# Optimization experiments

Hardware: AMD Instinct MI355X
Metric: run time of the kernel (lower is better)

The kernel has to match this reference:

```python
import jax, jax.numpy as jnp
import numpy as np

P = 8192  # num_particles
C = 8192  # num EEG channels (must equal P for the original broadcast to be valid)


def setup_inputs() -> dict:
    key = jax.random.key(0)
    k1, k2, k3, k4, k5 = jax.random.split(key, 5)
    inputs = jax.random.normal(k1, (1, C, P), dtype=jnp.float32)
    state_vector = jax.random.normal(k2, (P, 3), dtype=jnp.float32)
    # near-identity transition for numerical sanity
    transition_matrix = jnp.eye(3, dtype=jnp.float32) + 0.01 * jax.random.normal(k3, (3, 3), dtype=jnp.float32)
    # symmetric positive-definite process noise covariance (Cholesky must succeed)
    a = jax.random.normal(k4, (3, 3), dtype=jnp.float32)
    process_noise_cov = 0.01 * (a @ a.T) + 0.1 * jnp.eye(3, dtype=jnp.float32)
    forward_matrix = jax.random.normal(k5, (C, 3), dtype=jnp.float32)
    return {
        "inputs": inputs,
        "state_vector": state_vector,
        "transition_matrix": transition_matrix,
        "process_noise_cov": process_noise_cov,
        "forward_matrix": forward_matrix,
    }


def reference(inputs, state_vector, transition_matrix, process_noise_cov, forward_matrix):
    k_noise, k_cat = jax.random.split(jax.random.key(42))
    # --- state transition: x_new = x @ T^T + eps,  eps ~ N(0, Q) via z @ chol(Q) ---
    updated = state_vector @ transition_matrix.T                      # (P, 3)
    L = jnp.linalg.cholesky(process_noise_cov)                        # (3, 3) lower
    z = jax.random.normal(k_noise, (P, 3), dtype=state_vector.dtype)
    state = updated + z @ L                                           # (P, 3)
    # --- EEG measurement model: H @ x^T -> (C, P) ---
    predicted = forward_matrix @ state.T                              # (C, P)
    # --- particle weights: squared-residual sum (broadcast (1,C,P) - (P,C), C==P) ---
    w = jnp.sum(jnp.square(inputs - predicted.T), axis=-1)[0]         # (P,)
    # --- categorical resampling on log-weights (unnormalized logits) ---
    idx = jax.random.categorical(k_cat, jnp.log(w), shape=(P,))       # (P,) int
    resampled = state[idx]                                            # (P, 3) gather
    return jnp.mean(resampled, axis=0)                                # (3,)
```

## Files before the change

### kernel.cpp

```cpp
#include <hip/hip_runtime.h>
#include <stdint.h>

#define NP 8192
#define NC 8192

__host__ __device__ inline uint32_t rotl32(uint32_t x, int r) {
  return (x << r) | (x >> (32 - r));
}

__host__ __device__ inline void threefry2x32(uint32_t k0, uint32_t k1,
                                             uint32_t x0, uint32_t x1,
                                             uint32_t& o0, uint32_t& o1) {
  uint32_t ks2 = k0 ^ k1 ^ 0x1BD11BDAu;
  x0 += k0; x1 += k1;
#define TF_R(r) { x0 += x1; x1 = rotl32(x1, (r)); x1 ^= x0; }
  TF_R(13) TF_R(15) TF_R(26) TF_R(6)   x0 += k1;  x1 += ks2 + 1u;
  TF_R(17) TF_R(29) TF_R(16) TF_R(24)  x0 += ks2; x1 += k0 + 2u;
  TF_R(13) TF_R(15) TF_R(26) TF_R(6)   x0 += k0;  x1 += k1 + 3u;
  TF_R(17) TF_R(29) TF_R(16) TF_R(24)  x0 += k1;  x1 += ks2 + 4u;
  TF_R(13) TF_R(15) TF_R(26) TF_R(6)   x0 += ks2; x1 += k0 + 5u;
#undef TF_R
  o0 = x0; o1 = x1;
}

__device__ inline uint32_t tf_bits(uint32_t k0, uint32_t k1, uint32_t i) {
  uint32_t o0, o1;
  threefry2x32(k0, k1, 0u, i, o0, o1);
  return o0 ^ o1;
}

__device__ inline float u01(uint32_t bits) {
  return __uint_as_float((bits >> 9) | 0x3f800000u) - 1.0f;
}

__device__ inline float erfinvf_(float x) {
  float w = -log1pf(-x * x);
  float p;
  if (w < 5.0f) {
    w -= 2.5f;
    p = 2.81022636e-08f;
    p = fmaf(p, w, 3.43273939e-07f);
    p = fmaf(p, w, -3.5233877e-06f);
    p = fmaf(p, w, -4.39150654e-06f);
    p = fmaf(p, w, 0.00021858087f);
    p = fmaf(p, w, -0.00125372503f);
    p = fmaf(p, w, -0.00417768164f);
    p = fmaf(p, w, 0.246640727f);
    p = fmaf(p, w, 1.50140941f);
  } else {
    w = sqrtf(w) - 3.0f;
    p = -0.000200214257f;
    p = fmaf(p, w, 0.000100950558f);
    p = fmaf(p, w, 0.00134934322f);
    p = fmaf(p, w, -0.00367342844f);
    p = fmaf(p, w, 0.00573950773f);
    p = fmaf(p, w, -0.0076224613f);
    p = fmaf(p, w, 0.00943887047f);
    p = fmaf(p, w, 1.00167406f);
    p = fmaf(p, w, 2.83297682f);
  }
  return p * x;
}

__global__ void __launch_bounds__(256) k_normal(uint32_t k0, uint32_t k1, float* __restrict__ z) {
  uint32_t j = blockIdx.x * blockDim.x + threadIdx.x;
  if (j >= NP * 3) return;
  uint32_t bits = tf_bits(k0, k1, j);
  const float lo = -0.99999994f;
  float v = fmaxf(lo, u01(bits) * 2.0f + lo);
  z[j] = 1.41421356f * erfinvf_(v);
}

__global__ void __launch_bounds__(256) k_state(const float* __restrict__ sv,
                                               const float* __restrict__ T,
                                               const float* __restrict__ Q,
                                               const float* __restrict__ z,
                                               float* __restrict__ st) {
  int i = blockIdx.x * blockDim.x + threadIdx.x;
  if (i >= NP) return;
  float L00 = sqrtf(Q[0]);
  float L10 = Q[3] / L00, L20 = Q[6] / L00;
  float L11 = sqrtf(Q[4] - L10 * L10);
  float L21 = (Q[7] - L20 * L10) / L11;
  float L22 = sqrtf(Q[8] - L20 * L20 - L21 * L21);
  float s0 = sv[i * 3], s1 = sv[i * 3 + 1], s2 = sv[i * 3 + 2];
  float z0 = z[i * 3], z1 = z[i * 3 + 1], z2 = z[i * 3 + 2];
  float u0 = s0 * T[0] + s1 * T[1] + s2 * T[2];
  float u1 = s0 * T[3] + s1 * T[4] + s2 * T[5];
  float u2 = s0 * T[6] + s1 * T[7] + s2 * T[8];
  st[i * 3]     = u0 + (z0 * L00 + z1 * L10 + z2 * L20);
  st[i * 3 + 1] = u1 + (z1 * L11 + z2 * L21);
  st[i * 3 + 2] = u2 + (z2 * L22);
}

__global__ void __launch_bounds__(256) k_weights(const float* __restrict__ in,
                                                 const float* __restrict__ H,
                                                 const float* __restrict__ st,
                                                 float* __restrict__ winv) {
  int wave = threadIdx.x >> 6;
  int lane = threadIdx.x & 63;
  int row = blockIdx.x * 4 + wave;
  float s0 = st[row * 3], s1 = st[row * 3 + 1], s2 = st[row * 3 + 2];
  const float4* inrow = (const float4*)(in + (size_t)row * NC);
  const float4* H4 = (const float4*)H;
  float acc = 0.0f;
#pragma unroll 8
  for (int it = lane; it < NC / 4; it += 64) {
    float4 x = inrow[it];
    float4 h0 = H4[it * 3 + 0];
    float4 h1 = H4[it * 3 + 1];
    float4 h2 = H4[it * 3 + 2];
    float p0 = h0.x * s0 + h0.y * s1 + h0.z * s2;
    float p1 = h0.w * s0 + h1.x * s1 + h1.y * s2;
    float p2 = h1.z * s0 + h1.w * s1 + h2.x * s2;
    float p3 = h2.y * s0 + h2.z * s1 + h2.w * s2;
    float d0 = x.x - p0, d1 = x.y - p1, d2 = x.z - p2, d3 = x.w - p3;
    acc += d0 * d0 + d1 * d1 + d2 * d2 + d3 * d3;
  }
#pragma unroll
  for (int off = 32; off > 0; off >>= 1) acc += __shfl_down(acc, off, 64);
  if (lane == 0) winv[row] = 1.0f / acc;
}

__global__ void __launch_bounds__(256) k_resample(uint32_t k0, uint32_t k1,
                                                  const float* __restrict__ winv,
                                                  int* __restrict__ idx) {
  __shared__ float wi[NP];
  for (int t = threadIdx.x; t < NP; t += 256) wi[t] = winv[t];
  __syncthreads();
  uint32_t s = blockIdx.x;
  uint32_t base = s * (uint32_t)NP;
  const float TINY = 1.17549435e-38f;
  float best = 3.4e38f;
  int bi = 0;
#pragma unroll 4
  for (uint32_t i = threadIdx.x; i < NP; i += 256) {
    uint32_t bits = tf_bits(k0, k1, base + i);
    float v = fmaxf(TINY, u01(bits) + TINY);
    float y = -__logf(v);
    float r = y * wi[i];
    if (r < best) { best = r; bi = (int)i; }
  }
  __shared__ float rv[256];
  __shared__ int ri[256];
  rv[threadIdx.x] = best;
  ri[threadIdx.x] = bi;
  __syncthreads();
  for (int stp = 128; stp > 0; stp >>= 1) {
    if (threadIdx.x < stp) {
      float va = rv[threadIdx.x], vb = rv[threadIdx.x + stp];
      int ia = ri[threadIdx.x], ib = ri[threadIdx.x + stp];
      if (vb < va || (vb == va && ib < ia)) { rv[threadIdx.x] = vb; ri[threadIdx.x] = ib; }
    }
    __syncthreads();
  }
  if (threadIdx.x == 0) idx[s] = ri[0];
}

__global__ void __launch_bounds__(256) k_mean(const float* __restrict__ st,
                                              const int* __restrict__ idx,
                                              float* __restrict__ out) {
  double a0 = 0, a1 = 0, a2 = 0;
  for (int s = threadIdx.x; s < NP; s += 256) {
    int j = idx[s];
    a0 += st[j * 3];
    a1 += st[j * 3 + 1];
    a2 += st[j * 3 + 2];
  }
  __shared__ double r0[256], r1[256], r2[256];
  r0[threadIdx.x] = a0; r1[threadIdx.x] = a1; r2[threadIdx.x] = a2;
  __syncthreads();
  for (int s = 128; s > 0; s >>= 1) {
    if (threadIdx.x < s) {
      r0[threadIdx.x] += r0[threadIdx.x + s];
      r1[threadIdx.x] += r1[threadIdx.x + s];
      r2[threadIdx.x] += r2[threadIdx.x + s];
    }
    __syncthreads();
  }
  if (threadIdx.x == 0) {
    out[0] = (float)(r0[0] / NP);
    out[1] = (float)(r1[0] / NP);
    out[2] = (float)(r2[0] / NP);
  }
}

extern "C" void kernel_launch(void* const* d_in, const int* in_sizes, int n_in,
                              void* d_out, int out_size, void* d_ws, size_t ws_size,
                              hipStream_t stream) {
  const float* in = (const float*)d_in[0];
  const float* sv = (const float*)d_in[1];
  const float* T  = (const float*)d_in[2];
  const float* Q  = (const float*)d_in[3];
  const float* H  = (const float*)d_in[4];
  float* out = (float*)d_out;

  float* z    = (float*)d_ws;
  float* st   = z + 24576;
  float* winv = st + 24576;
  int*   idx  = (int*)(winv + NP);

  uint32_t nk0, nk1, ck0, ck1;
  threefry2x32(0u, 42u, 0u, 0u, nk0, nk1);
  threefry2x32(0u, 42u, 0u, 1u, ck0, ck1);

  hipLaunchKernelGGL(k_normal, dim3(96), dim3(256), 0, stream, nk0, nk1, z);
  hipLaunchKernelGGL(k_state, dim3(32), dim3(256), 0, stream, sv, T, Q, z, st);
  hipLaunchKernelGGL(k_weights, dim3(NP / 4), dim3(256), 0, stream, in, H, st, winv);
  hipLaunchKernelGGL(k_resample, dim3(NP), dim3(256), 0, stream, ck0, ck1, winv, idx);
  hipLaunchKernelGGL(k_mean, dim3(1), dim3(256), 0, stream, st, idx, out);
}
```

Measured before the change: 576.1 us.

## Fuse noise and state kernels, transpose H, drop shared weight staging

Merges the normal-noise generation and state transition into one prep kernel, which also writes a transposed copy of the forward matrix. The weights kernel can then read H as three contiguous planes instead of interleaved float4 triples. The resample kernel no longer stages the 32KB weight array in shared memory per block and reads it straight from global or cache. The mean kernel moves to 1024 threads, and the rotate uses a builtin. Changing the uniform clamp from max(TINY, u+TINY) to max(u, TINY) may shift results for very small uniforms.

```diff
diff --git a/kernel.cpp b/kernel.cpp
--- a/kernel.cpp
+++ b/kernel.cpp
@@ -5,7 +5,7 @@
 #define NC 8192
 
 __host__ __device__ inline uint32_t rotl32(uint32_t x, int r) {
-  return (x << r) | (x >> (32 - r));
+  return __builtin_rotateleft32(x, (unsigned)r);
 }
 
 __host__ __device__ inline void threefry2x32(uint32_t k0, uint32_t k1,
@@ -62,39 +62,45 @@
   return p * x;
 }
 
-__global__ void __launch_bounds__(256) k_normal(uint32_t k0, uint32_t k1, float* __restrict__ z) {
-  uint32_t j = blockIdx.x * blockDim.x + threadIdx.x;
-  if (j >= NP * 3) return;
-  uint32_t bits = tf_bits(k0, k1, j);
-  const float lo = -0.99999994f;
-  float v = fmaxf(lo, u01(bits) * 2.0f + lo);
-  z[j] = 1.41421356f * erfinvf_(v);
-}
-
-__global__ void __launch_bounds__(256) k_state(const float* __restrict__ sv,
-                                               const float* __restrict__ T,
-                                               const float* __restrict__ Q,
-                                               const float* __restrict__ z,
-                                               float* __restrict__ st) {
-  int i = blockIdx.x * blockDim.x + threadIdx.x;
-  if (i >= NP) return;
-  float L00 = sqrtf(Q[0]);
-  float L10 = Q[3] / L00, L20 = Q[6] / L00;
-  float L11 = sqrtf(Q[4] - L10 * L10);
-  float L21 = (Q[7] - L20 * L10) / L11;
-  float L22 = sqrtf(Q[8] - L20 * L20 - L21 * L21);
-  float s0 = sv[i * 3], s1 = sv[i * 3 + 1], s2 = sv[i * 3 + 2];
-  float z0 = z[i * 3], z1 = z[i * 3 + 1], z2 = z[i * 3 + 2];
-  float u0 = s0 * T[0] + s1 * T[1] + s2 * T[2];
-  float u1 = s0 * T[3] + s1 * T[4] + s2 * T[5];
-  float u2 = s0 * T[6] + s1 * T[7] + s2 * T[8];
-  st[i * 3]     = u0 + (z0 * L00 + z1 * L10 + z2 * L20);
-  st[i * 3 + 1] = u1 + (z1 * L11 + z2 * L21);
-  st[i * 3 + 2] = u2 + (z2 * L22);
+__global__ void __launch_bounds__(256) k_prep(uint32_t k0, uint32_t k1,
+                                              const float* __restrict__ sv,
+                                              const float* __restrict__ T,
+                                              const float* __restrict__ Q,
+                                              const float* __restrict__ H,
+                                              float* __restrict__ st,
+                                              float* __restrict__ ht) {
+  int b = blockIdx.x;
+  if (b < 32) {
+    int i = b * 256 + threadIdx.x;
+    const float lo = -0.99999994f;
+    float zz[3];
+#pragma unroll
+    for (int k = 0; k < 3; k++) {
+      uint32_t bits = tf_bits(k0, k1, 3u * (uint32_t)i + (uint32_t)k);
+      float v = fmaxf(lo, u01(bits) * 2.0f + lo);
+      zz[k] = 1.41421356f * erfinvf_(v);
+    }
+    float L00 = sqrtf(Q[0]);
+    float L10 = Q[3] / L00, L20 = Q[6] / L00;
+    float L11 = sqrtf(Q[4] - L10 * L10);
+    float L21 = (Q[7] - L20 * L10) / L11;
+    float L22 = sqrtf(Q[8] - L20 * L20 - L21 * L21);
+    float s0 = sv[i * 3], s1 = sv[i * 3 + 1], s2 = sv[i * 3 + 2];
+    float u0 = s0 * T[0] + s1 * T[1] + s2 * T[2];
+    float u1 = s0 * T[3] + s1 * T[4] + s2 * T[5];
+    float u2 = s0 * T[6] + s1 * T[7] + s2 * T[8];
+    st[i * 3]     = u0 + (zz[0] * L00 + zz[1] * L10 + zz[2] * L20);
+    st[i * 3 + 1] = u1 + (zz[1] * L11 + zz[2] * L21);
+    st[i * 3 + 2] = u2 + (zz[2] * L22);
+  } else {
+    int t = (b - 32) * 256 + threadIdx.x;
+    int k = t >> 13, j = t & (NP - 1);
+    ht[t] = H[j * 3 + k];
+  }
 }
 
 __global__ void __launch_bounds__(256) k_weights(const float* __restrict__ in,
-                                                 const float* __restrict__ H,
+                                                 const float* __restrict__ ht,
                                                  const float* __restrict__ st,
                                                  float* __restrict__ winv) {
   int wave = threadIdx.x >> 6;
@@ -102,19 +108,20 @@
   int row = blockIdx.x * 4 + wave;
   float s0 = st[row * 3], s1 = st[row * 3 + 1], s2 = st[row * 3 + 2];
   const float4* inrow = (const float4*)(in + (size_t)row * NC);
-  const float4* H4 = (const float4*)H;
+  const float4* h0 = (const float4*)ht;
+  const float4* h1 = (const float4*)(ht + NC);
+  const float4* h2 = (const float4*)(ht + 2 * NC);
   float acc = 0.0f;
-#pragma unroll 8
+#pragma unroll 4
   for (int it = lane; it < NC / 4; it += 64) {
     float4 x = inrow[it];
-    float4 h0 = H4[it * 3 + 0];
-    float4 h1 = H4[it * 3 + 1];
-    float4 h2 = H4[it * 3 + 2];
-    float p0 = h0.x * s0 + h0.y * s1 + h0.z * s2;
-    float p1 = h0.w * s0 + h1.x * s1 + h1.y * s2;
-    float p2 = h1.z * s0 + h1.w * s1 + h2.x * s2;
-    float p3 = h2.y * s0 + h2.z * s1 + h2.w * s2;
-    float d0 = x.x - p0, d1 = x.y - p1, d2 = x.z - p2, d3 = x.w - p3;
+    float4 a = h0[it];
+    float4 b = h1[it];
+    float4 c = h2[it];
+    float d0 = x.x - (a.x * s0 + b.x * s1 + c.x * s2);
+    float d1 = x.y - (a.y * s0 + b.y * s1 + c.y * s2);
+    float d2 = x.z - (a.z * s0 + b.z * s1 + c.z * s2);
+    float d3 = x.w - (a.w * s0 + b.w * s1 + c.w * s2);
     acc += d0 * d0 + d1 * d1 + d2 * d2 + d3 * d3;
   }
 #pragma unroll
@@ -125,9 +132,6 @@
 __global__ void __launch_bounds__(256) k_resample(uint32_t k0, uint32_t k1,
                                                   const float* __restrict__ winv,
                                                   int* __restrict__ idx) {
-  __shared__ float wi[NP];
-  for (int t = threadIdx.x; t < NP; t += 256) wi[t] = winv[t];
-  __syncthreads();
   uint32_t s = blockIdx.x;
   uint32_t base = s * (uint32_t)NP;
   const float TINY = 1.17549435e-38f;
@@ -136,9 +140,8 @@
 #pragma unroll 4
   for (uint32_t i = threadIdx.x; i < NP; i += 256) {
     uint32_t bits = tf_bits(k0, k1, base + i);
-    float v = fmaxf(TINY, u01(bits) + TINY);
-    float y = -__logf(v);
-    float r = y * wi[i];
+    float v = fmaxf(u01(bits), TINY);
+    float r = -__logf(v) * winv[i];
     if (r < best) { best = r; bi = (int)i; }
   }
   __shared__ float rv[256];
@@ -157,20 +160,20 @@
   if (threadIdx.x == 0) idx[s] = ri[0];
 }
 
-__global__ void __launch_bounds__(256) k_mean(const float* __restrict__ st,
-                                              const int* __restrict__ idx,
-                                              float* __restrict__ out) {
+__global__ void __launch_bounds__(1024) k_mean(const float* __restrict__ st,
+                                               const int* __restrict__ idx,
+                                               float* __restrict__ out) {
   double a0 = 0, a1 = 0, a2 = 0;
-  for (int s = threadIdx.x; s < NP; s += 256) {
+  for (int s = threadIdx.x; s < NP; s += 1024) {
     int j = idx[s];
     a0 += st[j * 3];
     a1 += st[j * 3 + 1];
     a2 += st[j * 3 + 2];
   }
-  __shared__ double r0[256], r1[256], r2[256];
+  __shared__ double r0[1024], r1[1024], r2[1024];
   r0[threadIdx.x] = a0; r1[threadIdx.x] = a1; r2[threadIdx.x] = a2;
   __syncthreads();
-  for (int s = 128; s > 0; s >>= 1) {
+  for (int s = 512; s > 0; s >>= 1) {
     if (threadIdx.x < s) {
       r0[threadIdx.x] += r0[threadIdx.x + s];
       r1[threadIdx.x] += r1[threadIdx.x + s];
@@ -195,18 +198,17 @@
   const float* H  = (const float*)d_in[4];
   float* out = (float*)d_out;
 
-  float* z    = (float*)d_ws;
-  float* st   = z + 24576;
-  float* winv = st + 24576;
+  float* st   = (float*)d_ws;
+  float* ht   = st + 24576;
+  float* winv = ht + 24576;
   int*   idx  = (int*)(winv + NP);
 
   uint32_t nk0, nk1, ck0, ck1;
   threefry2x32(0u, 42u, 0u, 0u, nk0, nk1);
   threefry2x32(0u, 42u, 0u, 1u, ck0, ck1);
 
-  hipLaunchKernelGGL(k_normal, dim3(96), dim3(256), 0, stream, nk0, nk1, z);
-  hipLaunchKernelGGL(k_state, dim3(32), dim3(256), 0, stream, sv, T, Q, z, st);
-  hipLaunchKernelGGL(k_weights, dim3(NP / 4), dim3(256), 0, stream, in, H, st, winv);
+  hipLaunchKernelGGL(k_prep, dim3(128), dim3(256), 0, stream, nk0, nk1, sv, T, Q, H, st, ht);
+  hipLaunchKernelGGL(k_weights, dim3(NP / 4), dim3(256), 0, stream, in, ht, st, winv);
   hipLaunchKernelGGL(k_resample, dim3(NP), dim3(256), 0, stream, ck0, ck1, winv, idx);
-  hipLaunchKernelGGL(k_mean, dim3(1), dim3(256), 0, stream, st, idx, out);
-}
+  hipLaunchKernelGGL(k_mean, dim3(1), dim3(1024), 0, stream, st, idx, out);
+}
```

After: 563.6 us. 1.02x faster.
